# Kernel tuning notes

Hardware: AMD Instinct MI355X
Metric: run time of the kernel (lower is better)

## Reference

```python
import jax, jax.numpy as jnp
import numpy as np

D_MODEL = 2048
N_HEADS = 16
HEAD_DIM = D_MODEL // N_HEADS


def setup_inputs() -> dict:
    key = jax.random.key(0)
    ks = jax.random.split(key, 5)
    b, l, d = 2, 2048, D_MODEL
    x = jax.random.normal(ks[0], (b, l, d), dtype=jnp.float32)
    # torch nn.Linear weights: y = x @ W.T + b, W shape [out, in]
    s_qkv = 1.0 / np.sqrt(d)
    W_qkv = jax.random.uniform(ks[1], (3 * d, d), dtype=jnp.float32, minval=-s_qkv, maxval=s_qkv)
    b_qkv = jax.random.uniform(ks[2], (3 * d,), dtype=jnp.float32, minval=-s_qkv, maxval=s_qkv)
    W_out = jax.random.uniform(ks[3], (d, d), dtype=jnp.float32, minval=-s_qkv, maxval=s_qkv)
    b_out = jax.random.uniform(ks[4], (d,), dtype=jnp.float32, minval=-s_qkv, maxval=s_qkv)
    return {"x": x, "W_qkv": W_qkv, "b_qkv": b_qkv, "W_out": W_out, "b_out": b_out}


def reference(x, W_qkv, b_qkv, W_out, b_out):
    b, l, d = x.shape
    h, e = N_HEADS, HEAD_DIM
    qkv = x @ W_qkv.T + b_qkv                      # [b, l, 3d]
    q, k, v = jnp.split(qkv, 3, axis=-1)
    # split heads: [b, l, h, e]
    q = q.reshape(b, l, h, e)
    k = k.reshape(b, l, h, e)
    v = v.reshape(b, l, h, e)
    scale = 1.0 / jnp.sqrt(jnp.float32(e))
    scores = jnp.einsum('bqhe,bkhe->bhqk', q, k) * scale  # [b, h, l, l]
    # causal mask (is_causal=True)
    causal = jnp.tril(jnp.ones((l, l), dtype=bool))
    scores = jnp.where(causal[None, None], scores, -jnp.inf)
    attn = jax.nn.softmax(scores, axis=-1)          # dropout p=0 -> identity
    out = jnp.einsum('bhqk,bkhe->bqhe', attn, v)    # [b, l, h, e]
    out = out.reshape(b, l, d)                      # merge heads
    out = out @ W_out.T + b_out
    return out
```

## Files before the change

kernel.cpp:

```cpp
#include <hip/hip_runtime.h>
#include <hip/hip_bf16.h>

#define B_ 2
#define L_ 2048
#define D_ 2048
#define H_ 16
#define E_ 128
#define M_ 4096
#define K_ 2048
#define N3_ 6144

typedef __attribute__((ext_vector_type(4))) float f32x4;
typedef short s16x8 __attribute__((ext_vector_type(8)));

__device__ inline void gld_lds16(const void* g, void* l) {
    __builtin_amdgcn_global_load_lds(
        (const __attribute__((address_space(1))) void*)g,
        (__attribute__((address_space(3))) void*)l, 16, 0, 0);
}

__global__ __launch_bounds__(256)
void cast_bf16(const float* __restrict__ in, __hip_bfloat16* __restrict__ out, int n8)
{
    const int i = blockIdx.x * 256 + threadIdx.x;
    if (i >= n8) return;
    const float4 a = ((const float4*)in)[2 * i];
    const float4 b = ((const float4*)in)[2 * i + 1];
    union { __hip_bfloat16 h[8]; uint4 u; } o;
    o.h[0] = __float2bfloat16(a.x); o.h[1] = __float2bfloat16(a.y);
    o.h[2] = __float2bfloat16(a.z); o.h[3] = __float2bfloat16(a.w);
    o.h[4] = __float2bfloat16(b.x); o.h[5] = __float2bfloat16(b.y);
    o.h[6] = __float2bfloat16(b.z); o.h[7] = __float2bfloat16(b.w);
    ((uint4*)out)[i] = o.u;
}

__global__ __launch_bounds__(256)
void gemm_bf16_nt(const __hip_bfloat16* __restrict__ A,
                  const __hip_bfloat16* __restrict__ W,
                  const float* __restrict__ bias,
                  __hip_bfloat16* __restrict__ q,
                  __hip_bfloat16* __restrict__ k,
                  __hip_bfloat16* __restrict__ vT,
                  float* __restrict__ o,
                  const int mode)
{
    __shared__ __hip_bfloat16 As[128 * 32];
    __shared__ __hip_bfloat16 Bs[128 * 32];

    const int t    = threadIdx.x;
    const int lane = t & 63;
    const int w    = t >> 6;
    const int l15  = lane & 15;
    const int hi   = lane >> 4;
    const int wr   = w >> 1, wc = w & 1;
    const int m0   = blockIdx.y << 7;
    const int n0   = blockIdx.x << 7;

    f32x4 acc[4][4];
    const f32x4 z4 = {0.f, 0.f, 0.f, 0.f};
    #pragma unroll
    for (int m = 0; m < 4; ++m)
        #pragma unroll
        for (int n = 0; n < 4; ++n) acc[m][n] = z4;

    const __hip_bfloat16* Ab = A + (size_t)m0 * K_;
    const __hip_bfloat16* Bb = W + (size_t)n0 * K_;
    const int srow = t >> 2;
    const int sc   = (t & 3) << 3;

    for (int k0 = 0; k0 < K_; k0 += 32) {
        #pragma unroll
        for (int j = 0; j < 2; ++j) {
            gld_lds16(Ab + (size_t)(j * 64 + srow) * K_ + k0 + sc,
                      (char*)As + j * 4096 + w * 1024);
            gld_lds16(Bb + (size_t)(j * 64 + srow) * K_ + k0 + sc,
                      (char*)Bs + j * 4096 + w * 1024);
        }
        __syncthreads();
        s16x8 af[4], bf[4];
        #pragma unroll
        for (int m = 0; m < 4; ++m)
            af[m] = *(const s16x8*)(As + (wr * 64 + m * 16 + l15) * 32 + hi * 8);
        #pragma unroll
        for (int n = 0; n < 4; ++n)
            bf[n] = *(const s16x8*)(Bs + (wc * 64 + n * 16 + l15) * 32 + hi * 8);
        #pragma unroll
        for (int m = 0; m < 4; ++m)
            #pragma unroll
            for (int n = 0; n < 4; ++n)
                acc[m][n] = __builtin_amdgcn_mfma_f32_16x16x32_bf16(af[m], bf[n], acc[m][n], 0, 0, 0);
        __syncthreads();
    }

    if (mode == 1) {
        #pragma unroll
        for (int n = 0; n < 4; ++n) {
            const int col = n0 + wc * 64 + n * 16 + l15;
            const float bn = bias[col];
            #pragma unroll
            for (int m = 0; m < 4; ++m) {
                const int rowb = m0 + wr * 64 + m * 16 + hi * 4;
                #pragma unroll
                for (int i = 0; i < 4; ++i)
                    o[(size_t)(rowb + i) * D_ + col] = acc[m][n][i] + bn;
            }
        }
    } else {
        const int which = n0 >> 11;
        const int h     = (n0 >> 7) & 15;
        #pragma unroll
        for (int n = 0; n < 4; ++n) {
            const int e  = wc * 64 + n * 16 + l15;
            const float bn = bias[n0 + e];
            #pragma unroll
            for (int m = 0; m < 4; ++m) {
                const int rowb = m0 + wr * 64 + m * 16 + hi * 4;
                #pragma unroll
                for (int i = 0; i < 4; ++i) {
                    const int mm = rowb + i;
                    const int b  = mm >> 11;
                    const int l  = mm & 2047;
                    const __hip_bfloat16 val = __float2bfloat16(acc[m][n][i] + bn);
                    if (which == 0)
                        q[((size_t)((b * H_ + h) * L_ + l) << 7) + e] = val;
                    else if (which == 1)
                        k[((size_t)((b * H_ + h) * L_ + l) << 7) + e] = val;
                    else
                        vT[(((size_t)(b * H_ + h) << 7) + e) * L_ + l] = val;
                }
            }
        }
    }
}

__global__ __launch_bounds__(256)
void attn_mfma(const __hip_bfloat16* __restrict__ Qg,
               const __hip_bfloat16* __restrict__ Kg,
               const __hip_bfloat16* __restrict__ vTg,
               __hip_bfloat16* __restrict__ O)
{
    __shared__ __hip_bfloat16 Ks[2][64 * 128];
    __shared__ __hip_bfloat16 Vt[2][128 * 64];
    __shared__ __hip_bfloat16 Ps[4 * 1024];

    const int t    = threadIdx.x;
    const int lane = t & 63;
    const int w    = t >> 6;
    const int l15  = lane & 15;
    const int hi   = lane >> 4;
    const int pq   = blockIdx.x;
    const int bh   = blockIdx.y;
    const size_t base = (size_t)bh * (L_ * E_);
    const float scale = 0.08838834764831843f;
    const int krow = t >> 4;
    const int kc16 = t & 15;

    const __hip_bfloat16* Kbh  = Kg  + base;
    const __hip_bfloat16* vTbh = vTg + base;

    auto stage = [&](int kt2, int buf) {
        const __hip_bfloat16* Kb = Kbh + ((size_t)(kt2 << 6)) * E_;
        char* kd = (char*)Ks + buf * 16384 + (w << 10);
        #pragma unroll
        for (int j = 0; j < 4; ++j) {
            const int row = (j << 4) + krow;
            const int csw = kc16 ^ (row & 7);
            gld_lds16(Kb + (size_t)row * E_ + (csw << 3), kd + (j << 12));
        }
        const __hip_bfloat16* Vb = vTbh + (kt2 << 6);
        char* vd = (char*)Vt + buf * 16384 + (w << 10);
        #pragma unroll
        for (int j = 0; j < 4; ++j) {
            const int e  = (j << 5) + (t >> 3);
            const int g8 = (t & 7) ^ (e & 7);
            gld_lds16(Vb + (size_t)e * L_ + (g8 << 3), vd + (j << 12));
        }
    };

    const f32x4 z4 = {0.f, 0.f, 0.f, 0.f};

    #pragma unroll 1
    for (int seg = 0; seg < 2; ++seg) {
        const int qt = seg ? pq : 31 - pq;
        const int q0 = (qt << 6) + (w << 4);

        s16x8 qf[4];
        #pragma unroll
        for (int e0 = 0; e0 < 4; ++e0)
            qf[e0] = *(const s16x8*)(Qg + base + (size_t)(q0 + l15) * E_ + e0 * 32 + hi * 8);

        f32x4 oacc[8];
        #pragma unroll
        for (int ef = 0; ef < 8; ++ef) oacc[ef] = z4;
        float mrow[4] = {-1e30f, -1e30f, -1e30f, -1e30f};
        float lrow[4] = {0.f, 0.f, 0.f, 0.f};

        stage(0, 0);
        __syncthreads();

        for (int kt = 0; kt <= qt; ++kt) {
            const int cur = kt & 1;
            if (kt < qt) stage(kt + 1, cur ^ 1);

            const char* Ksc = (const char*)Ks + cur * 16384;
            const char* Vtc = (const char*)Vt + cur * 16384;

            f32x4 sf[4];
            #pragma unroll
            for (int c = 0; c < 4; ++c) {
                f32x4 s = z4;
                const int row = (c << 4) + l15;
                #pragma unroll
                for (int e0 = 0; e0 < 4; ++e0) {
                    const int ch = ((e0 << 2) + hi) ^ (row & 7);
                    const s16x8 kf = *(const s16x8*)(Ksc + (row << 8) + (ch << 4));
                    s = __builtin_amdgcn_mfma_f32_16x16x32_bf16(qf[e0], kf, s, 0, 0, 0);
                }
                sf[c] = s;
            }

            float p4[4][4];
            float tmax[4] = {-1e30f, -1e30f, -1e30f, -1e30f};
            if (kt == qt) {
                const int qg = q0 + (hi << 2);
                #pragma unroll
                for (int c = 0; c < 4; ++c) {
                    const int kvg = (kt << 6) + (c << 4) + l15;
                    #pragma unroll
                    for (int i = 0; i < 4; ++i) {
                        float s = sf[c][i] * scale;
                        if (kvg > qg + i) s = -1e30f;
                        p4[c][i] = s;
                        tmax[i] = fmaxf(tmax[i], s);
                    }
                }
            } else {
                #pragma unroll
                for (int c = 0; c < 4; ++c)
                    #pragma unroll
                    for (int i = 0; i < 4; ++i) {
                        const float s = sf[c][i] * scale;
                        p4[c][i] = s;
                        tmax[i] = fmaxf(tmax[i], s);
                    }
            }
            float fsc[4];
            #pragma unroll
            for (int i = 0; i < 4; ++i) {
                float v = tmax[i];
                v = fmaxf(v, __shfl_xor(v, 1));
                v = fmaxf(v, __shfl_xor(v, 2));
                v = fmaxf(v, __shfl_xor(v, 4));
                v = fmaxf(v, __shfl_xor(v, 8));
                const float mnew = fmaxf(mrow[i], v);
                fsc[i] = __expf(mrow[i] - mnew);
                mrow[i] = mnew;
                float sum = 0.f;
                #pragma unroll
                for (int c = 0; c < 4; ++c) {
                    const float pe = __expf(p4[c][i] - mnew);
                    p4[c][i] = pe;
                    sum += pe;
                }
                sum += __shfl_xor(sum, 1);
                sum += __shfl_xor(sum, 2);
                sum += __shfl_xor(sum, 4);
                sum += __shfl_xor(sum, 8);
                lrow[i] = lrow[i] * fsc[i] + sum;
            }
            #pragma unroll
            for (int ef = 0; ef < 8; ++ef)
                #pragma unroll
                for (int i = 0; i < 4; ++i) oacc[ef][i] *= fsc[i];

            #pragma unroll
            for (int c = 0; c < 4; ++c)
                #pragma unroll
                for (int i = 0; i < 4; ++i) {
                    const int r   = (hi << 2) + i;
                    const int col = (c << 4) + l15;
                    const int ch  = (col >> 3) ^ (r & 7);
                    const int by  = (r << 7) + ((ch << 4) | ((col & 7) << 1));
                    *(__hip_bfloat16*)((char*)Ps + (w << 11) + by) = __float2bfloat16(p4[c][i]);
                }
            asm volatile("s_waitcnt lgkmcnt(0)" ::: "memory");

            #pragma unroll
            for (int kh = 0; kh < 2; ++kh) {
                const int chp = ((kh << 2) + hi) ^ (l15 & 7);
                const s16x8 pa = *(const s16x8*)((char*)Ps + (w << 11) + (l15 << 7) + (chp << 4));
                #pragma unroll
                for (int ef = 0; ef < 8; ++ef) {
                    const int e   = (ef << 4) + l15;
                    const int chv = ((kh << 2) + hi) ^ (e & 7);
                    const s16x8 vb = *(const s16x8*)(Vtc + (e << 7) + (chv << 4));
                    oacc[ef] = __builtin_amdgcn_mfma_f32_16x16x32_bf16(pa, vb, oacc[ef], 0, 0, 0);
                }
            }
            __syncthreads();
        }

        const int b = bh >> 4, h = bh & 15;
        float invl[4];
        #pragma unroll
        for (int i = 0; i < 4; ++i) invl[i] = 1.f / lrow[i];
        #pragma unroll
        for (int ef = 0; ef < 8; ++ef) {
            const int e = (ef << 4) + l15;
            #pragma unroll
            for (int i = 0; i < 4; ++i) {
                const int row = q0 + (hi << 2) + i;
                O[((size_t)(b * L_ + row) * D_) + (h << 7) + e] =
                    __float2bfloat16(oacc[ef][i] * invl[i]);
            }
        }
    }
}

extern "C" void kernel_launch(void* const* d_in, const int* in_sizes, int n_in,
                              void* d_out, int out_size, void* d_ws, size_t ws_size,
                              hipStream_t stream)
{
    const float* x    = (const float*)d_in[0];
    const float* Wqkv = (const float*)d_in[1];
    const float* bqkv = (const float*)d_in[2];
    const float* Wout = (const float*)d_in[3];
    const float* bout = (const float*)d_in[4];
    float* out = (float*)d_out;

    __hip_bfloat16* xb  = (__hip_bfloat16*)d_ws;
    __hip_bfloat16* wqb = xb  + (size_t)M_ * K_;
    __hip_bfloat16* wob = wqb + (size_t)N3_ * K_;
    __hip_bfloat16* qb  = wob + (size_t)D_ * K_;
    __hip_bfloat16* kb  = qb  + (size_t)M_ * D_;
    __hip_bfloat16* vtb = kb  + (size_t)M_ * D_;
    __hip_bfloat16* aob = vtb + (size_t)M_ * D_;

    cast_bf16<<<(M_ * K_ / 8) / 256, 256, 0, stream>>>(x, xb, M_ * K_ / 8);
    cast_bf16<<<(N3_ * K_ / 8) / 256, 256, 0, stream>>>(Wqkv, wqb, N3_ * K_ / 8);
    cast_bf16<<<(D_ * K_ / 8) / 256, 256, 0, stream>>>(Wout, wob, D_ * K_ / 8);

    dim3 blk(256);
    dim3 g1(N3_ / 128, M_ / 128);
    gemm_bf16_nt<<<g1, blk, 0, stream>>>(xb, wqb, bqkv, qb, kb, vtb, nullptr, 0);

    dim3 g2(16, B_ * H_);
    attn_mfma<<<g2, blk, 0, stream>>>(qb, kb, vtb, aob);

    dim3 g3(D_ / 128, M_ / 128);
    gemm_bf16_nt<<<g3, blk, 0, stream>>>(aob, wob, bout, nullptr, nullptr, nullptr, out, 1);
}
```

Measured before the change: 447.0 us.

## Pipeline GEMM with double-buffered swizzled LDS, lazy softmax rescale, fused casts

The GEMM kernel is replaced by a 512-thread, 128x256-tile kernel. It uses double-buffered XOR-swizzled LDS, a K step of 64, prefetch issued between two MFMA half-phases, and s_setprio around the MFMA blocks, so global loads overlap compute. The attention softmax skips the max reduction and output rescale unless a row max grows by more than 8, and it defers the row-sum shuffle reduction to the end. The three cast launches are merged into one kernel. Risks include lower occupancy from the larger LDS footprint, grid underfill for the output projection (8x32 blocks), and the fixed-threshold lazy rescale, which is exact because the stored max is updated whenever the bound is exceeded.

```diff
diff --git a/kernel.cpp b/kernel.cpp
--- a/kernel.cpp
+++ b/kernel.cpp
@@ -20,117 +20,173 @@
 }
 
 __global__ __launch_bounds__(256)
-void cast_bf16(const float* __restrict__ in, __hip_bfloat16* __restrict__ out, int n8)
+void cast3_bf16(const float* __restrict__ a, __hip_bfloat16* __restrict__ ao, int na,
+                const float* __restrict__ b, __hip_bfloat16* __restrict__ bo, int nb,
+                const float* __restrict__ c, __hip_bfloat16* __restrict__ co, int nc)
 {
     const int i = blockIdx.x * 256 + threadIdx.x;
-    if (i >= n8) return;
-    const float4 a = ((const float4*)in)[2 * i];
-    const float4 b = ((const float4*)in)[2 * i + 1];
+    const float* in; __hip_bfloat16* out; int j;
+    if (i < na)                { in = a; out = ao; j = i; }
+    else if (i < na + nb)      { in = b; out = bo; j = i - na; }
+    else if (i < na + nb + nc) { in = c; out = co; j = i - na - nb; }
+    else return;
+    const float4 x = ((const float4*)in)[2 * j];
+    const float4 y = ((const float4*)in)[2 * j + 1];
     union { __hip_bfloat16 h[8]; uint4 u; } o;
-    o.h[0] = __float2bfloat16(a.x); o.h[1] = __float2bfloat16(a.y);
-    o.h[2] = __float2bfloat16(a.z); o.h[3] = __float2bfloat16(a.w);
-    o.h[4] = __float2bfloat16(b.x); o.h[5] = __float2bfloat16(b.y);
-    o.h[6] = __float2bfloat16(b.z); o.h[7] = __float2bfloat16(b.w);
-    ((uint4*)out)[i] = o.u;
+    o.h[0] = __float2bfloat16(x.x); o.h[1] = __float2bfloat16(x.y);
+    o.h[2] = __float2bfloat16(x.z); o.h[3] = __float2bfloat16(x.w);
+    o.h[4] = __float2bfloat16(y.x); o.h[5] = __float2bfloat16(y.y);
+    o.h[6] = __float2bfloat16(y.z); o.h[7] = __float2bfloat16(y.w);
+    ((uint4*)out)[j] = o.u;
 }
 
-__global__ __launch_bounds__(256)
-void gemm_bf16_nt(const __hip_bfloat16* __restrict__ A,
-                  const __hip_bfloat16* __restrict__ W,
-                  const float* __restrict__ bias,
-                  __hip_bfloat16* __restrict__ q,
-                  __hip_bfloat16* __restrict__ k,
-                  __hip_bfloat16* __restrict__ vT,
-                  float* __restrict__ o,
-                  const int mode)
+__global__ __launch_bounds__(512, 2)
+void gemm_nt_2ph(const __hip_bfloat16* __restrict__ A,
+                 const __hip_bfloat16* __restrict__ W,
+                 const float* __restrict__ bias,
+                 __hip_bfloat16* __restrict__ q,
+                 __hip_bfloat16* __restrict__ k,
+                 __hip_bfloat16* __restrict__ vT,
+                 float* __restrict__ o,
+                 const int mode)
 {
-    __shared__ __hip_bfloat16 As[128 * 32];
-    __shared__ __hip_bfloat16 Bs[128 * 32];
+    __shared__ char lds[98304];
 
     const int t    = threadIdx.x;
     const int lane = t & 63;
     const int w    = t >> 6;
     const int l15  = lane & 15;
     const int hi   = lane >> 4;
-    const int wr   = w >> 1, wc = w & 1;
+    const int wr   = w >> 2;
+    const int wc   = w & 3;
+    const int n0   = blockIdx.x << 8;
     const int m0   = blockIdx.y << 7;
-    const int n0   = blockIdx.x << 7;
-
-    f32x4 acc[4][4];
+
+    f32x4 acc[2][4][2];
     const f32x4 z4 = {0.f, 0.f, 0.f, 0.f};
     #pragma unroll
-    for (int m = 0; m < 4; ++m)
-        #pragma unroll
-        for (int n = 0; n < 4; ++n) acc[m][n] = z4;
-
-    const __hip_bfloat16* Ab = A + (size_t)m0 * K_;
-    const __hip_bfloat16* Bb = W + (size_t)n0 * K_;
-    const int srow = t >> 2;
-    const int sc   = (t & 3) << 3;
-
-    for (int k0 = 0; k0 < K_; k0 += 32) {
-        #pragma unroll
-        for (int j = 0; j < 2; ++j) {
-            gld_lds16(Ab + (size_t)(j * 64 + srow) * K_ + k0 + sc,
-                      (char*)As + j * 4096 + w * 1024);
-            gld_lds16(Bb + (size_t)(j * 64 + srow) * K_ + k0 + sc,
-                      (char*)Bs + j * 4096 + w * 1024);
-        }
-        __syncthreads();
-        s16x8 af[4], bf[4];
+    for (int hf = 0; hf < 2; ++hf)
         #pragma unroll
         for (int m = 0; m < 4; ++m)
-            af[m] = *(const s16x8*)(As + (wr * 64 + m * 16 + l15) * 32 + hi * 8);
-        #pragma unroll
-        for (int n = 0; n < 4; ++n)
-            bf[n] = *(const s16x8*)(Bs + (wc * 64 + n * 16 + l15) * 32 + hi * 8);
-        #pragma unroll
-        for (int m = 0; m < 4; ++m)
-            #pragma unroll
-            for (int n = 0; n < 4; ++n)
-                acc[m][n] = __builtin_amdgcn_mfma_f32_16x16x32_bf16(af[m], bf[n], acc[m][n], 0, 0, 0);
-        __syncthreads();
+            #pragma unroll
+            for (int n = 0; n < 2; ++n) acc[hf][m][n] = z4;
+
+    s16x8 afr[4][2], bfr[2][2];
+
+    const __hip_bfloat16* Abase = A + (size_t)m0 * K_;
+    const __hip_bfloat16* Wbase = W + (size_t)n0 * K_;
+
+    auto stage_half = [&](const __hip_bfloat16* src, char* dst) {
+        #pragma unroll
+        for (int i = 0; i < 2; ++i) {
+            const int slot = (i << 9) + t;
+            const int row  = slot >> 3;
+            const int csw  = (slot & 7) ^ (row & 7);
+            gld_lds16(src + (size_t)row * K_ + (csw << 3),
+                      dst + (i << 13) + (w << 10));
+        }
+    };
+
+    stage_half(Abase,                     lds);
+    stage_half(Wbase,                     lds + 16384);
+    stage_half(Wbase + (size_t)128 * K_,  lds + 32768);
+    asm volatile("s_waitcnt vmcnt(2)" ::: "memory");
+    __builtin_amdgcn_s_barrier();
+
+    const int NT = K_ / 64;
+    for (int T = 0; T < NT; ++T) {
+        const char* Lc = lds + (T & 1) * 49152;
+        char*       Ln = lds + ((T & 1) ^ 1) * 49152;
+        const __hip_bfloat16* Asrc = Abase + (size_t)(T + 1) * 64;
+        const __hip_bfloat16* Wsrc = Wbase + (size_t)(T + 1) * 64;
+        const bool pf = (T + 1 < NT);
+
+        auto lda = [&](int m, int kk) {
+            const int r  = (wr << 6) + (m << 4) + l15;
+            const int ch = ((kk << 2) + hi) ^ (r & 7);
+            return *(const s16x8*)(Lc + r * 128 + (ch << 4));
+        };
+        auto ldb = [&](int reg, int n, int kk) {
+            const int r  = (wc << 5) + (n << 4) + l15;
+            const int ch = ((kk << 2) + hi) ^ (r & 7);
+            return *(const s16x8*)(Lc + reg + r * 128 + (ch << 4));
+        };
+
+        #pragma unroll
+        for (int m = 0; m < 4; ++m) { afr[m][0] = lda(m, 0); afr[m][1] = lda(m, 1); }
+        #pragma unroll
+        for (int n = 0; n < 2; ++n) { bfr[n][0] = ldb(16384, n, 0); bfr[n][1] = ldb(16384, n, 1); }
+        if (pf) { stage_half(Asrc, Ln); stage_half(Wsrc, Ln + 16384); }
+        __builtin_amdgcn_s_barrier();
+        __builtin_amdgcn_s_setprio(1);
+        #pragma unroll
+        for (int kk = 0; kk < 2; ++kk)
+            #pragma unroll
+            for (int n = 0; n < 2; ++n)
+                #pragma unroll
+                for (int m = 0; m < 4; ++m)
+                    acc[0][m][n] = __builtin_amdgcn_mfma_f32_16x16x32_bf16(
+                        afr[m][kk], bfr[n][kk], acc[0][m][n], 0, 0, 0);
+        __builtin_amdgcn_s_setprio(0);
+        if (pf) asm volatile("s_waitcnt vmcnt(4)" ::: "memory");
+        else    asm volatile("s_waitcnt vmcnt(0)" ::: "memory");
+        __builtin_amdgcn_s_barrier();
+
+        #pragma unroll
+        for (int n = 0; n < 2; ++n) { bfr[n][0] = ldb(32768, n, 0); bfr[n][1] = ldb(32768, n, 1); }
+        if (pf) stage_half(Wsrc + (size_t)128 * K_, Ln + 32768);
+        __builtin_amdgcn_s_barrier();
+        __builtin_amdgcn_s_setprio(1);
+        #pragma unroll
+        for (int kk = 0; kk < 2; ++kk)
+            #pragma unroll
+            for (int n = 0; n < 2; ++n)
+                #pragma unroll
+                for (int m = 0; m < 4; ++m)
+                    acc[1][m][n] = __builtin_amdgcn_mfma_f32_16x16x32_bf16(
+                        afr[m][kk], bfr[n][kk], acc[1][m][n], 0, 0, 0);
+        __builtin_amdgcn_s_setprio(0);
+        asm volatile("s_waitcnt vmcnt(2)" ::: "memory");
+        __builtin_amdgcn_s_barrier();
     }
 
-    if (mode == 1) {
-        #pragma unroll
-        for (int n = 0; n < 4; ++n) {
-            const int col = n0 + wc * 64 + n * 16 + l15;
+    #pragma unroll
+    for (int hf = 0; hf < 2; ++hf)
+        #pragma unroll
+        for (int n = 0; n < 2; ++n) {
+            const int col  = n0 + (hf << 7) + (wc << 5) + (n << 4) + l15;
             const float bn = bias[col];
-            #pragma unroll
-            for (int m = 0; m < 4; ++m) {
-                const int rowb = m0 + wr * 64 + m * 16 + hi * 4;
-                #pragma unroll
-                for (int i = 0; i < 4; ++i)
-                    o[(size_t)(rowb + i) * D_ + col] = acc[m][n][i] + bn;
-            }
-        }
-    } else {
-        const int which = n0 >> 11;
-        const int h     = (n0 >> 7) & 15;
-        #pragma unroll
-        for (int n = 0; n < 4; ++n) {
-            const int e  = wc * 64 + n * 16 + l15;
-            const float bn = bias[n0 + e];
-            #pragma unroll
-            for (int m = 0; m < 4; ++m) {
-                const int rowb = m0 + wr * 64 + m * 16 + hi * 4;
-                #pragma unroll
-                for (int i = 0; i < 4; ++i) {
-                    const int mm = rowb + i;
-                    const int b  = mm >> 11;
-                    const int l  = mm & 2047;
-                    const __hip_bfloat16 val = __float2bfloat16(acc[m][n][i] + bn);
-                    if (which == 0)
-                        q[((size_t)((b * H_ + h) * L_ + l) << 7) + e] = val;
-                    else if (which == 1)
-                        k[((size_t)((b * H_ + h) * L_ + l) << 7) + e] = val;
-                    else
-                        vT[(((size_t)(b * H_ + h) << 7) + e) * L_ + l] = val;
-                }
-            }
-        }
-    }
+            if (mode == 1) {
+                #pragma unroll
+                for (int m = 0; m < 4; ++m) {
+                    const int rowb = m0 + (wr << 6) + (m << 4) + (hi << 2);
+                    #pragma unroll
+                    for (int i = 0; i < 4; ++i)
+                        o[(size_t)(rowb + i) * D_ + col] = acc[hf][m][n][i] + bn;
+                }
+            } else {
+                const int which = col >> 11;
+                const int h     = (col >> 7) & 15;
+                const int e     = col & 127;
+                #pragma unroll
+                for (int m = 0; m < 4; ++m) {
+                    const int rowb = m0 + (wr << 6) + (m << 4) + (hi << 2);
+                    #pragma unroll
+                    for (int i = 0; i < 4; ++i) {
+                        const int mm = rowb + i;
+                        const int b  = mm >> 11;
+                        const int l  = mm & 2047;
+                        const __hip_bfloat16 val = __float2bfloat16(acc[hf][m][n][i] + bn);
+                        if (which == 0)
+                            q[((size_t)((b * H_ + h) * L_ + l) << 7) + e] = val;
+                        else if (which == 1)
+                            k[((size_t)((b * H_ + h) * L_ + l) << 7) + e] = val;
+                        else
+                            vT[(((size_t)(b * H_ + h) << 7) + e) * L_ + l] = val;
+                    }
+                }
+            }
+        }
 }
 
 __global__ __launch_bounds__(256)
@@ -193,7 +249,7 @@
         #pragma unroll
         for (int ef = 0; ef < 8; ++ef) oacc[ef] = z4;
         float mrow[4] = {-1e30f, -1e30f, -1e30f, -1e30f};
-        float lrow[4] = {0.f, 0.f, 0.f, 0.f};
+        float lsum[4] = {0.f, 0.f, 0.f, 0.f};
 
         stage(0, 0);
         __syncthreads();
@@ -244,34 +300,34 @@
                         tmax[i] = fmaxf(tmax[i], s);
                     }
             }
-            float fsc[4];
-            #pragma unroll
-            for (int i = 0; i < 4; ++i) {
-                float v = tmax[i];
-                v = fmaxf(v, __shfl_xor(v, 1));
-                v = fmaxf(v, __shfl_xor(v, 2));
-                v = fmaxf(v, __shfl_xor(v, 4));
-                v = fmaxf(v, __shfl_xor(v, 8));
-                const float mnew = fmaxf(mrow[i], v);
-                fsc[i] = __expf(mrow[i] - mnew);
-                mrow[i] = mnew;
-                float sum = 0.f;
+
+            int ok = 1;
+            #pragma unroll
+            for (int i = 0; i < 4; ++i) ok &= (tmax[i] <= mrow[i] + 8.f);
+            if (!__all(ok)) {
+                #pragma unroll
+                for (int i = 0; i < 4; ++i) {
+                    float v = tmax[i];
+                    v = fmaxf(v, __shfl_xor(v, 1));
+                    v = fmaxf(v, __shfl_xor(v, 2));
+                    v = fmaxf(v, __shfl_xor(v, 4));
+                    v = fmaxf(v, __shfl_xor(v, 8));
+                    const float mnew = fmaxf(mrow[i], v);
+                    const float fsc  = __expf(mrow[i] - mnew);
+                    mrow[i] = mnew;
+                    lsum[i] *= fsc;
+                    #pragma unroll
+                    for (int ef = 0; ef < 8; ++ef) oacc[ef][i] *= fsc;
+                }
+            }
+            #pragma unroll
+            for (int i = 0; i < 4; ++i)
                 #pragma unroll
                 for (int c = 0; c < 4; ++c) {
-                    const float pe = __expf(p4[c][i] - mnew);
+                    const float pe = __expf(p4[c][i] - mrow[i]);
                     p4[c][i] = pe;
-                    sum += pe;
-                }
-                sum += __shfl_xor(sum, 1);
-                sum += __shfl_xor(sum, 2);
-                sum += __shfl_xor(sum, 4);
-                sum += __shfl_xor(sum, 8);
-                lrow[i] = lrow[i] * fsc[i] + sum;
-            }
-            #pragma unroll
-            for (int ef = 0; ef < 8; ++ef)
-                #pragma unroll
-                for (int i = 0; i < 4; ++i) oacc[ef][i] *= fsc[i];
+                    lsum[i] += pe;
+                }
 
             #pragma unroll
             for (int c = 0; c < 4; ++c)
@@ -300,10 +356,17 @@
             __syncthreads();
         }
 
+        float invl[4];
+        #pragma unroll
+        for (int i = 0; i < 4; ++i) {
+            float s = lsum[i];
+            s += __shfl_xor(s, 1);
+            s += __shfl_xor(s, 2);
+            s += __shfl_xor(s, 4);
+            s += __shfl_xor(s, 8);
+            invl[i] = 1.f / s;
+        }
         const int b = bh >> 4, h = bh & 15;
-        float invl[4];
-        #pragma unroll
-        for (int i = 0; i < 4; ++i) invl[i] = 1.f / lrow[i];
         #pragma unroll
         for (int ef = 0; ef < 8; ++ef) {
             const int e = (ef << 4) + l15;
@@ -336,17 +399,15 @@
     __hip_bfloat16* vtb = kb  + (size_t)M_ * D_;
     __hip_bfloat16* aob = vtb + (size_t)M_ * D_;
 
-    cast_bf16<<<(M_ * K_ / 8) / 256, 256, 0, stream>>>(x, xb, M_ * K_ / 8);
-    cast_bf16<<<(N3_ * K_ / 8) / 256, 256, 0, stream>>>(Wqkv, wqb, N3_ * K_ / 8);
-    cast_bf16<<<(D_ * K_ / 8) / 256, 256, 0, stream>>>(Wout, wob, D_ * K_ / 8);
-
-    dim3 blk(256);
-    dim3 g1(N3_ / 128, M_ / 128);
-    gemm_bf16_nt<<<g1, blk, 0, stream>>>(xb, wqb, bqkv, qb, kb, vtb, nullptr, 0);
+    const int na = M_ * K_ / 8, nb = N3_ * K_ / 8, nc = D_ * K_ / 8;
+    cast3_bf16<<<(na + nb + nc) / 256, 256, 0, stream>>>(x, xb, na, Wqkv, wqb, nb, Wout, wob, nc);
+
+    dim3 g1(N3_ / 256, M_ / 128);
+    gemm_nt_2ph<<<g1, dim3(512), 0, stream>>>(xb, wqb, bqkv, qb, kb, vtb, nullptr, 0);
 
     dim3 g2(16, B_ * H_);
-    attn_mfma<<<g2, blk, 0, stream>>>(qb, kb, vtb, aob);
-
-    dim3 g3(D_ / 128, M_ / 128);
-    gemm_bf16_nt<<<g3, blk, 0, stream>>>(aob, wob, bout, nullptr, nullptr, nullptr, out, 1);
+    attn_mfma<<<g2, dim3(256), 0, stream>>>(qb, kb, vtb, aob);
+
+    dim3 g3(D_ / 256, M_ / 128);
+    gemm_nt_2ph<<<g3, dim3(512), 0, stream>>>(aob, wob, bout, nullptr, nullptr, nullptr, out, 1);
 }
```

Measured after the change: 389.9 us. 1.15x faster.
